# Kernel optimization log

Hardware: AMD Instinct MI355X
Metric: run time of the kernel (lower is better)

The kernel has to match this reference:

```python
import jax, jax.numpy as jnp
import numpy as np

B, CIN, L = 4, 128, 2048
D_MODEL, D_STATE, EXPAND, HEADDIM, NGROUPS = 256, 16, 3, 3, 1
D_INNER = EXPAND * D_MODEL            # 768
NHEADS = D_INNER // HEADDIM           # 256
CONV_DIM = D_INNER + 2 * NGROUPS * D_STATE   # 800
D_IN_PROJ = 2 * D_INNER + 2 * NGROUPS * D_STATE + NHEADS  # 1824
K_PROJ, D_CONV = 4, 4
EPS = 1e-5


def setup_inputs() -> dict:
    key = jax.random.key(0)
    ks = jax.random.split(key, 9)
    x = jax.random.normal(ks[0], (B, CIN, L), jnp.float32)
    proj_w = jax.random.normal(ks[1], (D_MODEL, CIN, K_PROJ), jnp.float32) / np.float32(np.sqrt(CIN * K_PROJ))
    in_proj_w = jax.random.normal(ks[2], (D_IN_PROJ, D_MODEL), jnp.float32) / np.float32(np.sqrt(D_MODEL))
    conv_w = jax.random.normal(ks[3], (CONV_DIM, 1, D_CONV), jnp.float32) / np.float32(np.sqrt(D_CONV))
    conv_b = jax.random.normal(ks[4], (CONV_DIM,), jnp.float32) * 0.01
    # dt_bias = inverse-softplus of dt ~ LogUniform[1e-3, 1e-1] (mamba2 init)
    u = jax.random.uniform(ks[5], (NHEADS,), jnp.float32)
    dt = jnp.exp(u * np.float32(np.log(0.1) - np.log(1e-3)) + np.float32(np.log(1e-3)))
    dt_bias = dt + jnp.log(-jnp.expm1(-dt))
    A_log = jnp.log(1.0 + 15.0 * jax.random.uniform(ks[6], (NHEADS,), jnp.float32))  # A in [-16,-1]
    D_skip = jnp.ones((NHEADS,), jnp.float32)
    norm_w = jnp.ones((D_INNER,), jnp.float32)
    out_proj_w = jax.random.normal(ks[7], (D_MODEL, D_INNER), jnp.float32) / np.float32(np.sqrt(D_INNER))
    return {"x": x, "proj_w": proj_w, "in_proj_w": in_proj_w, "conv_w": conv_w,
            "conv_b": conv_b, "dt_bias": dt_bias, "A_log": A_log, "D_skip": D_skip,
            "norm_w": norm_w, "out_proj_w": out_proj_w}


def _forward(x, proj_w, in_proj_w, conv_w, conv_b, dt_bias, A_log, D_skip, norm_w, out_proj_w):
    # outer Conv1d, padding='same' (k=4 -> left 1, right 2), no bias: (B,CIN,L)->(B,D_MODEL,L)
    h = jax.lax.conv_general_dilated(x, proj_w, (1,), [(1, 2)],
                                     dimension_numbers=("NCH", "OIH", "NCH"))
    u = h.transpose(0, 2, 1)                          # (B, L, d_model)
    zxbcdt = jnp.einsum("bld,ed->ble", u, in_proj_w)  # (B, L, 1824)
    z = zxbcdt[..., :D_INNER]                                     # (B,L,768)
    xBC = zxbcdt[..., D_INNER:D_INNER + CONV_DIM]                 # (B,L,800)
    dt = zxbcdt[..., D_INNER + CONV_DIM:]                         # (B,L,256)
    dt = jax.nn.softplus(dt + dt_bias)
    # depthwise causal conv (pad d_conv-1 on left) + SiLU
    xBC_c = jax.lax.conv_general_dilated(xBC.transpose(0, 2, 1), conv_w, (1,), [(D_CONV - 1, 0)],
                                         feature_group_count=CONV_DIM,
                                         dimension_numbers=("NCH", "OIH", "NCH"))
    xBC = jax.nn.silu(xBC_c + conv_b[None, :, None]).transpose(0, 2, 1)  # (B,L,800)
    xs = xBC[..., :D_INNER].reshape(B, L, NHEADS, HEADDIM)        # (B,L,H,P)
    Bm = xBC[..., D_INNER:D_INNER + D_STATE]                      # (B,L,N) (ngroups=1)
    Cm = xBC[..., D_INNER + D_STATE:]                             # (B,L,N)
    A = -jnp.exp(A_log)                                           # (H,)

    def step(hst, inp):
        dt_t, x_t, B_t, C_t = inp                 # (B,H),(B,H,P),(B,N),(B,N)
        dA = jnp.exp(dt_t * A)[:, :, None, None]  # (B,H,1,1)
        hst = dA * hst + jnp.einsum("bh,bhp,bn->bhpn", dt_t, x_t, B_t)
        y_t = jnp.einsum("bhpn,bn->bhp", hst, C_t)
        return hst, y_t

    h0 = jnp.zeros((B, NHEADS, HEADDIM, D_STATE), x.dtype)
    _, ys = jax.lax.scan(step, h0, (dt.transpose(1, 0, 2), xs.transpose(1, 0, 2, 3),
                                    Bm.transpose(1, 0, 2), Cm.transpose(1, 0, 2)))
    y = ys.transpose(1, 0, 2, 3) + D_skip[None, None, :, None] * xs   # (B,L,H,P)
    y = y.reshape(B, L, D_INNER)
    # gated RMSNorm: gate first, then normalize (norm_before_gate=False)
    y = y * jax.nn.silu(z)
    y = y * jax.lax.rsqrt(jnp.mean(y * y, axis=-1, keepdims=True) + EPS) * norm_w
    out = jnp.einsum("ble,de->bld", y, out_proj_w)   # (B,L,d_model)
    return out.transpose(0, 2, 1)                    # (B,d_model,L)


def reference(x, proj_w, in_proj_w, conv_w, conv_b, dt_bias, A_log, D_skip, norm_w, out_proj_w):
    return _forward(x, proj_w, in_proj_w, conv_w, conv_b, dt_bias, A_log, D_skip, norm_w, out_proj_w)
```

## Files before the change

### kernel.cpp

```cpp
#include <hip/hip_runtime.h>
#include <hip/hip_fp16.h>
#include <math.h>

#define B_     4
#define CIN    128
#define LEN    2048
#define DMODEL 256
#define DSTATE 16
#define NHEADS 256
#define DINNER 768
#define CONVDIM 800
#define DINPROJ 1824
#define EPS_   1e-5f
#define BAND   64
#define NBAND  32

typedef _Float16 f16x8 __attribute__((ext_vector_type(8)));
typedef _Float16 f16x4 __attribute__((ext_vector_type(4)));
typedef float    f32x4 __attribute__((ext_vector_type(4)));

__device__ __forceinline__ float silu_(float x){ return x / (1.0f + __expf(-x)); }
__device__ __forceinline__ float softplus_(float x){
    return x > 0.f ? x + log1pf(__expf(-x)) : log1pf(__expf(x));
}

__device__ __forceinline__ void gl2lds16(const _Float16* g, _Float16* l){
    __builtin_amdgcn_global_load_lds(
        (const __attribute__((address_space(1))) void*)g,
        (__attribute__((address_space(3))) void*)l, 16, 0, 0);
}

__global__ __launch_bounds__(256) void k_f2h(const float* __restrict__ a,
                                             _Float16* __restrict__ o, int n){
    for (int i = blockIdx.x * 256 + threadIdx.x; i < n; i += gridDim.x * 256)
        o[i] = (_Float16)a[i];
}

__global__ __launch_bounds__(256) void k_im2col(const float* __restrict__ x,
                                                _Float16* __restrict__ xcol){
    __shared__ float xs[CIN][68];
    int blk = blockIdx.x;
    int b  = blk >> 5;
    int l0 = (blk & 31) << 6;
    const float* xb = x + (size_t)b * CIN * LEN;
    for (int idx = threadIdx.x; idx < CIN * 67; idx += 256){
        int ci = idx / 67, j = idx % 67;
        int gl = l0 - 1 + j;
        xs[ci][j] = (gl >= 0 && gl < LEN) ? xb[ci * LEN + gl] : 0.f;
    }
    __syncthreads();
    #pragma unroll
    for (int v = 0; v < 16; v++){
        int id = v * 256 + threadIdx.x;
        int rl = id >> 6, c = id & 63;
        f16x8 pk;
        #pragma unroll
        for (int e = 0; e < 8; e++){
            int ci = c * 2 + (e >> 2), k = e & 3;
            pk[e] = (_Float16)xs[ci][rl + k];
        }
        *(f16x8*)&xcol[((size_t)(b * LEN + l0 + rl)) * 512 + c * 8] = pk;
    }
}

template<int K, int EPI>
__global__ __launch_bounds__(256) void k_gemm(const _Float16* __restrict__ A,
                                              const _Float16* __restrict__ Bw,
                                              const float* __restrict__ dt_bias,
                                              _Float16* __restrict__ o_u,
                                              _Float16* __restrict__ o_z,
                                              _Float16* __restrict__ o_xbc,
                                              _Float16* __restrict__ o_dt,
                                              float* __restrict__ o_f){
    __shared__ __align__(16) _Float16 As[128 * 32];
    __shared__ __align__(16) _Float16 Bs[128 * 32];
    int tid  = threadIdx.x;
    int wv   = tid >> 6;
    int lane = tid & 63;
    int quad = lane >> 4;
    int l16  = lane & 15;
    int m0 = blockIdx.x * 128;
    int n0 = blockIdx.y * 128;
    int wm = (wv >> 1) * 64;
    int wn = (wv & 1) * 64;
    int srow = lane >> 2;
    int scol = (lane & 3) * 8;

    f32x4 acc[4][4];
    #pragma unroll
    for (int i = 0; i < 4; i++)
        #pragma unroll
        for (int j = 0; j < 4; j++)
            acc[i][j] = (f32x4){0.f, 0.f, 0.f, 0.f};

    for (int k0 = 0; k0 < K; k0 += 32){
        #pragma unroll
        for (int j = 0; j < 2; j++){
            int ar = m0 + wv * 32 + j * 16 + srow;
            gl2lds16(A + (size_t)ar * K + k0 + scol,
                     &As[(wv * 32 + j * 16) * 32]);
            int nr = n0 + wv * 32 + j * 16 + srow;
            if (EPI == 1) nr = nr > (DINPROJ - 1) ? (DINPROJ - 1) : nr;
            gl2lds16(Bw + (size_t)nr * K + k0 + scol,
                     &Bs[(wv * 32 + j * 16) * 32]);
        }
        __syncthreads();
        f16x8 af[4], bf[4];
        #pragma unroll
        for (int i = 0; i < 4; i++)
            af[i] = *(const f16x8*)&As[(wm + i * 16 + l16) * 32 + quad * 8];
        #pragma unroll
        for (int j = 0; j < 4; j++)
            bf[j] = *(const f16x8*)&Bs[(wn + j * 16 + l16) * 32 + quad * 8];
        #pragma unroll
        for (int i = 0; i < 4; i++)
            #pragma unroll
            for (int j = 0; j < 4; j++)
                acc[i][j] = __builtin_amdgcn_mfma_f32_16x16x32_f16(
                                af[i], bf[j], acc[i][j], 0, 0, 0);
        __syncthreads();
    }

    if (EPI == 0){
        #pragma unroll
        for (int j = 0; j < 4; j++){
            int col = n0 + wn + j * 16 + l16;
            #pragma unroll
            for (int i = 0; i < 4; i++){
                int row = m0 + wm + i * 16 + quad * 4;
                #pragma unroll
                for (int r = 0; r < 4; r++)
                    o_u[(size_t)(row + r) * DMODEL + col] = (_Float16)acc[i][j][r];
            }
        }
    } else if (EPI == 1){
        #pragma unroll
        for (int j = 0; j < 4; j++){
            int col = n0 + wn + j * 16 + l16;
            if (col < DINNER){
                #pragma unroll
                for (int i = 0; i < 4; i++){
                    int row = m0 + wm + i * 16 + quad * 4;
                    #pragma unroll
                    for (int r = 0; r < 4; r++)
                        o_z[(size_t)(row + r) * DINNER + col] = (_Float16)acc[i][j][r];
                }
            } else if (col < DINNER + CONVDIM){
                int cc = col - DINNER;
                #pragma unroll
                for (int i = 0; i < 4; i++){
                    int row = m0 + wm + i * 16 + quad * 4;
                    #pragma unroll
                    for (int r = 0; r < 4; r++)
                        o_xbc[(size_t)(row + r) * CONVDIM + cc] = (_Float16)acc[i][j][r];
                }
            } else if (col < DINPROJ){
                int hh = col - (DINNER + CONVDIM);
                float bias = dt_bias[hh];
                #pragma unroll
                for (int i = 0; i < 4; i++){
                    int row = m0 + wm + i * 16 + quad * 4;
                    #pragma unroll
                    for (int r = 0; r < 4; r++)
                        o_dt[(size_t)(row + r) * NHEADS + hh] =
                            (_Float16)softplus_(acc[i][j][r] + bias);
                }
            }
        }
    } else {
        #pragma unroll
        for (int i = 0; i < 4; i++){
            int row = m0 + wm + i * 16 + quad * 4;
            int b = row >> 11, l = row & (LEN - 1);
            #pragma unroll
            for (int j = 0; j < 4; j++){
                int d = n0 + wn + j * 16 + l16;
                *(f32x4*)&o_f[(((size_t)(b * DMODEL + d)) << 11) + l] = acc[i][j];
            }
        }
    }
}

__global__ __launch_bounds__(256) void k_dwconv(const __half* __restrict__ xbc,
                                                const float* __restrict__ cw,
                                                const float* __restrict__ cb,
                                                __half* __restrict__ xcc){
    int idx = blockIdx.x * 256 + threadIdx.x;
    int c = idx % CONVDIM;
    int r = idx / CONVDIM;
    int l = r & (LEN - 1);
    float4 wv = *(const float4*)(cw + c * 4);
    float acc = cb[c];
    if (l >= 3){
        const __half* base = xbc + (size_t)(r - 3) * CONVDIM + c;
        acc += __half2float(base[0]) * wv.x + __half2float(base[CONVDIM]) * wv.y +
               __half2float(base[2 * CONVDIM]) * wv.z + __half2float(base[3 * CONVDIM]) * wv.w;
    } else {
        const float wk[4] = {wv.x, wv.y, wv.z, wv.w};
        for (int k = 0; k < 4; k++){
            int t = l - 3 + k;
            if (t >= 0) acc += __half2float(xbc[(size_t)(r + k - 3) * CONVDIM + c]) * wk[k];
        }
    }
    xcc[idx] = __float2half(silu_(acc));
}

__global__ __launch_bounds__(256) void k_y(const __half* __restrict__ dtb,
                                           const __half* __restrict__ xcc,
                                           const float* __restrict__ A_log,
                                           __half* __restrict__ y,
                                           float* __restrict__ E0,
                                           __half* __restrict__ cstate,
                                           float* __restrict__ dsum){
    __shared__ __align__(16) char smem[59392];
    __half* sBC = (__half*)smem;
    __half* sX  = (__half*)(smem + 4096);
    __half* sHL = (__half*)(smem + 4096);
    __half* sDT = (__half*)(smem + 28672);
    float*  sD  = (float*)(smem + 36864);
    float*  sG  = (float*)(smem + 54272);

    int band = blockIdx.x, hq = blockIdx.y, b = blockIdx.z;
    int row0 = band * BAND;
    int tid = threadIdx.x;
    int wv = tid >> 6, lane = tid & 63;

    {
        int c = wv, slot = c * 64 + lane;
        int row = slot >> 2, off = slot & 3;
        gl2lds16((const _Float16*)((const char*)xcc +
                   (size_t)(b * LEN + row0 + row) * 1600 + 1536 + off * 16),
                 (_Float16*)(smem + c * 1024));
    }
    #pragma unroll
    for (int i = 0; i < 6; i++){
        int c = wv + i * 4, slot = c * 64 + lane;
        int row = slot / 24, off = slot % 24;
        gl2lds16((const _Float16*)((const char*)xcc +
                   (size_t)(b * LEN + row0 + row) * 1600 + hq * 384 + off * 16),
                 (_Float16*)(smem + 4096 + c * 1024));
    }
    #pragma unroll
    for (int i = 0; i < 2; i++){
        int c = wv + i * 4, slot = c * 64 + lane;
        int row = slot >> 3, off = slot & 7;
        gl2lds16((const _Float16*)((const char*)dtb +
                   (size_t)(b * LEN + row0 + row) * 512 + hq * 128 + off * 16),
                 (_Float16*)(smem + 28672 + c * 1024));
    }
    __syncthreads();

    {
        int h = tid & 63, tb = tid >> 6;
        float A = -__expf(A_log[hq * 64 + h]);
        #pragma unroll
        for (int i = 0; i < 16; i++){
            int t = tb + i * 4;
            sD[t * 68 + h] = __expf(A * __half2float(sDT[t * 64 + h]));
        }
    }
    __syncthreads();

    if (tid < 64){
        int h = tid;
        float E = 1.f;
        float* ep = E0 + ((size_t)(b * LEN + row0)) * 256 + hq * 64 + h;
        for (int t = 0; t < 64; t++){
            E *= sD[t * 68 + h];
            *ep = E;
            ep += 256;
        }
        dsum[(size_t)(b * 256 + hq * 64 + h) * NBAND + band] = E;
    } else if (tid < 128){
        int tt = tid - 64;
        f16x8 ca = *(const f16x8*)&sBC[tt * 32 + 16];
        f16x8 cb = *(const f16x8*)&sBC[tt * 32 + 24];
        float cf[16];
        #pragma unroll
        for (int n = 0; n < 16; n++) cf[n] = (n < 8) ? (float)ca[n] : (float)cb[n - 8];
        for (int ss = 0; ss < 16; ss++){
            int s = (tt & 48) + ss;
            f16x8 ba = *(const f16x8*)&sBC[s * 32];
            f16x8 bb = *(const f16x8*)&sBC[s * 32 + 8];
            float acc = 0.f;
            #pragma unroll
            for (int n = 0; n < 8; n++)
                acc += cf[n] * (float)ba[n] + cf[n + 8] * (float)bb[n];
            sG[tt * 20 + ss] = acc;
        }
    } else {
        for (int idx = tid - 128; idx < 4096; idx += 128){
            int t = idx >> 6, h = idx & 63;
            float dtv = __half2float(sDT[t * 64 + h]);
            int xi = t * 192 + h * 3;
            sX[xi]     = __float2half(__half2float(sX[xi])     * dtv);
            sX[xi + 1] = __float2half(__half2float(sX[xi + 1]) * dtv);
            sX[xi + 2] = __float2half(__half2float(sX[xi + 2]) * dtv);
        }
    }
    __syncthreads();

    int t = tid >> 2, hsub = tid & 3, Hb = hsub * 16;
    int tmod = t & 15;
    float w[16], y0[16], y1[16], y2[16];
    #pragma unroll
    for (int i = 0; i < 16; i++){ w[i] = 1.f; y0[i] = 0.f; y1[i] = 0.f; y2[i] = 0.f; }

    for (int d = 0; d <= tmod; d++){
        int s = t - d;
        float g = sG[t * 20 + (tmod - d)];
        f32x4 Dv[4];
        #pragma unroll
        for (int k4 = 0; k4 < 4; k4++)
            Dv[k4] = *(const f32x4*)&sD[s * 68 + Hb + k4 * 4];
        f16x8 xv0 = *(const f16x8*)&sX[s * 192 + Hb * 3];
        f16x8 xv1 = *(const f16x8*)&sX[s * 192 + Hb * 3 + 8];
        f16x8 xv2 = *(const f16x8*)&sX[s * 192 + Hb * 3 + 16];
        f16x8 xv3 = *(const f16x8*)&sX[s * 192 + Hb * 3 + 24];
        f16x8 xv4 = *(const f16x8*)&sX[s * 192 + Hb * 3 + 32];
        f16x8 xv5 = *(const f16x8*)&sX[s * 192 + Hb * 3 + 40];
        #define XV(i) ((i)<8?(float)xv0[(i)]:(i)<16?(float)xv1[(i)-8]:(i)<24?(float)xv2[(i)-16]:\
                       (i)<32?(float)xv3[(i)-24]:(i)<40?(float)xv4[(i)-32]:(float)xv5[(i)-40])
        #pragma unroll
        for (int hh = 0; hh < 16; hh++){
            float wg = w[hh] * g;
            y0[hh] = fmaf(wg, XV(hh * 3 + 0), y0[hh]);
            y1[hh] = fmaf(wg, XV(hh * 3 + 1), y1[hh]);
            y2[hh] = fmaf(wg, XV(hh * 3 + 2), y2[hh]);
            w[hh] *= Dv[hh >> 2][hh & 3];
        }
        #undef XV
    }

    int h2 = tid >> 2, ng = tid & 3;
    float F[4][12];
    float vK[4];
    #pragma unroll
    for (int k = 0; k < 4; k++){
        #pragma unroll
        for (int i = 0; i < 12; i++) F[k][i] = 0.f;
        float v = 1.f;
        for (int ss = 15; ss >= 0; ss--){
            int s = k * 16 + ss;
            float x0 = __half2float(sX[s * 192 + h2 * 3]);
            float x1 = __half2float(sX[s * 192 + h2 * 3 + 1]);
            float x2 = __half2float(sX[s * 192 + h2 * 3 + 2]);
            f16x4 bv = *(const f16x4*)&sBC[s * 32 + ng * 4];
            #pragma unroll
            for (int nn = 0; nn < 4; nn++){
                float wb = v * (float)bv[nn];
                F[k][nn * 3 + 0] = fmaf(wb, x0, F[k][nn * 3 + 0]);
                F[k][nn * 3 + 1] = fmaf(wb, x1, F[k][nn * 3 + 1]);
                F[k][nn * 3 + 2] = fmaf(wb, x2, F[k][nn * 3 + 2]);
            }
            v *= sD[s * 68 + h2];
        }
        vK[k] = v;
    }

    __syncthreads();

    {
        float hc[12];
        #pragma unroll
        for (int i = 0; i < 12; i++) hc[i] = F[0][i];
        #pragma unroll
        for (int i = 0; i < 12; i++)
            sHL[(0 * 64 + h2) * 48 + ng * 12 + i] = __float2half(hc[i]);
        #pragma unroll
        for (int k = 1; k <= 2; k++){
            #pragma unroll
            for (int i = 0; i < 12; i++) hc[i] = fmaf(vK[k], hc[i], F[k][i]);
            #pragma unroll
            for (int i = 0; i < 12; i++)
                sHL[(k * 64 + h2) * 48 + ng * 12 + i] = __float2half(hc[i]);
        }
        __half* cp = cstate + ((size_t)((b * 256 + hq * 64 + h2) * NBAND + band)) * 48 + ng * 12;
        #pragma unroll
        for (int i = 0; i < 12; i++)
            cp[i] = __float2half(fmaf(vK[3], hc[i], F[3][i]));
    }
    __syncthreads();

    {
        f16x8 cva = *(const f16x8*)&sBC[t * 32 + 16];
        f16x8 cvb = *(const f16x8*)&sBC[t * 32 + 24];
        float cf[16];
        #pragma unroll
        for (int n = 0; n < 16; n++) cf[n] = (n < 8) ? (float)cva[n] : (float)cvb[n - 8];
        int k = t >> 4;
        if (k > 0){
            #pragma unroll
            for (int hh = 0; hh < 16; hh++){
                int h = Hb + hh;
                const __half* hl = &sHL[((k - 1) * 64 + h) * 48];
                f16x8 hv0 = *(const f16x8*)&hl[0];
                f16x8 hv1 = *(const f16x8*)&hl[8];
                f16x8 hv2 = *(const f16x8*)&hl[16];
                f16x8 hv3 = *(const f16x8*)&hl[24];
                f16x8 hv4 = *(const f16x8*)&hl[32];
                f16x8 hv5 = *(const f16x8*)&hl[40];
                #define HV(i) ((i)<8?(float)hv0[(i)]:(i)<16?(float)hv1[(i)-8]:(i)<24?(float)hv2[(i)-16]:\
                               (i)<32?(float)hv3[(i)-24]:(i)<40?(float)hv4[(i)-32]:(float)hv5[(i)-40])
                float a0 = 0.f, a1 = 0.f, a2 = 0.f;
                #pragma unroll
                for (int n = 0; n < 16; n++){
                    a0 = fmaf(cf[n], HV(n * 3 + 0), a0);
                    a1 = fmaf(cf[n], HV(n * 3 + 1), a1);
                    a2 = fmaf(cf[n], HV(n * 3 + 2), a2);
                }
                #undef HV
                y0[hh] = fmaf(w[hh], a0, y0[hh]);
                y1[hh] = fmaf(w[hh], a1, y1[hh]);
                y2[hh] = fmaf(w[hh], a2, y2[hh]);
            }
        }
        __half* yp = y + (size_t)(b * LEN + row0 + t) * DINNER + hq * 192 + hsub * 48;
        #pragma unroll
        for (int c = 0; c < 6; c++){
            f16x8 pk;
            #pragma unroll
            for (int e2 = 0; e2 < 8; e2++){
                int gi = c * 8 + e2;
                int hh = gi / 3, p = gi % 3;
                pk[e2] = (_Float16)(p == 0 ? y0[hh] : (p == 1 ? y1[hh] : y2[hh]));
            }
            *(f16x8*)&yp[c * 8] = pk;
        }
    }
}

__global__ __launch_bounds__(64) void k_scanB(__half* __restrict__ cstate,
                                              const float* __restrict__ dsum){
    int bh = blockIdx.x;
    int lane = threadIdx.x;
    if (lane >= 48) return;
    __half* st = cstate + (size_t)bh * NBAND * 48 + lane;
    const float* dd = dsum + (size_t)bh * NBAND;
    float H = 0.f;
    for (int c = 0; c < NBAND; c++){
        float d = dd[c];
        float s = __half2float(st[(size_t)c * 48]);
        st[(size_t)c * 48] = __float2half(H);
        H = fmaf(H, d, s);
    }
}

__global__ __launch_bounds__(256) void k_norm(__half* __restrict__ y,
                                              const __half* __restrict__ z,
                                              const __half* __restrict__ xcc,
                                              const float* __restrict__ E0,
                                              const __half* __restrict__ cstate,
                                              const float* __restrict__ D_skip,
                                              const float* __restrict__ nw){
    __shared__ __align__(16) char nsm[24576 + 64];
    __half* sHI = (__half*)nsm;
    float*  sCf = (float*)(nsm + 24576);
    __shared__ float wsum[4];
    int r = blockIdx.x;
    int b = r >> 11, l = r & (LEN - 1), band = l >> 6;
    int tid = threadIdx.x;
    int wv = tid >> 6, lane = tid & 63;

    #pragma unroll
    for (int i = 0; i < 6; i++){
        int chunk = (wv + i * 4) * 64 + lane;
        int head = chunk / 6, off = chunk % 6;
        gl2lds16((const _Float16*)((const char*)cstate +
                   ((size_t)(b * 256 + head) * NBAND + band) * 96 + off * 16),
                 (_Float16*)(nsm + (wv + i * 4) * 1024));
    }
    if (tid < 16)
        sCf[tid] = __half2float(xcc[(size_t)r * CONVDIM + DINNER + DSTATE + tid]);
    __syncthreads();

    const __half* zr = z + (size_t)r * DINNER;
    const __half* xr = xcc + (size_t)r * CONVDIM;
    const float*  er = E0 + (size_t)r * 256;
    __half* yr = y + (size_t)r * DINNER;
    float tv[3];
    #pragma unroll
    for (int q = 0; q < 3; q++){
        int e = tid + q * 256;
        int h = e / 3, p = e - h * 3;
        float corr = 0.f;
        #pragma unroll
        for (int n = 0; n < 16; n++)
            corr = fmaf(sCf[n], __half2float(sHI[h * 48 + n * 3 + p]), corr);
        float yf = __half2float(yr[e]) + er[h] * corr + D_skip[h] * __half2float(xr[e]);
        tv[q] = yf * silu_(__half2float(zr[e]));
    }
    float ss = tv[0] * tv[0] + tv[1] * tv[1] + tv[2] * tv[2];
    #pragma unroll
    for (int m = 1; m < 64; m <<= 1) ss += __shfl_xor(ss, m, 64);
    if ((tid & 63) == 0) wsum[tid >> 6] = ss;
    __syncthreads();
    float tot = wsum[0] + wsum[1] + wsum[2] + wsum[3];
    float sc = rsqrtf(tot / (float)DINNER + EPS_);
    #pragma unroll
    for (int q = 0; q < 3; q++){
        int e = tid + q * 256;
        yr[e] = __float2half(tv[q] * sc * nw[e]);
    }
}

extern "C" void kernel_launch(void* const* d_in, const int* in_sizes, int n_in,
                              void* d_out, int out_size, void* d_ws, size_t ws_size,
                              hipStream_t stream) {
    const float* x          = (const float*)d_in[0];
    const float* proj_w     = (const float*)d_in[1];
    const float* in_proj_w  = (const float*)d_in[2];
    const float* conv_w     = (const float*)d_in[3];
    const float* conv_b     = (const float*)d_in[4];
    const float* dt_bias    = (const float*)d_in[5];
    const float* A_log      = (const float*)d_in[6];
    const float* D_skip     = (const float*)d_in[7];
    const float* norm_w     = (const float*)d_in[8];
    const float* out_proj_w = (const float*)d_in[9];
    float* out = (float*)d_out;

    char* ob = (char*)d_out;
    _Float16* pw_h  = (_Float16*)ob;
    _Float16* ipw_h = (_Float16*)(ob + 262144);
    float*    E0    = (float*)d_out;

    char* wsb = (char*)d_ws;
    _Float16* xcol  = (_Float16*)(wsb);
    _Float16* u_h   = (_Float16*)(wsb + 8388608);
    __half*   xcc_h = (__half*)(wsb);
    __half*   z_h   = (__half*)(wsb + 13107200);
    __half*   xbc_h = (__half*)(wsb + 25690112);
    __half*   y_h   = xbc_h;
    __half*   dt_h  = (__half*)(wsb + 38797312);
    __half*   cstate= (__half*)(wsb + 42991616);
    float*    dsum  = (float*)(wsb + 46137344);
    _Float16* opw_h = (_Float16*)(wsb + 46268416);

    k_f2h   <<<64, 256, 0, stream>>>(proj_w,     pw_h,  DMODEL * CIN * 4);
    k_f2h   <<<64, 256, 0, stream>>>(in_proj_w,  ipw_h, DINPROJ * DMODEL);
    k_f2h   <<<64, 256, 0, stream>>>(out_proj_w, opw_h, DMODEL * DINNER);
    k_im2col<<<128, 256, 0, stream>>>(x, xcol);
    k_gemm<512, 0><<<dim3(64, 2), 256, 0, stream>>>(xcol, pw_h, nullptr,
        u_h, nullptr, nullptr, nullptr, nullptr);
    k_gemm<256, 1><<<dim3(64, 15), 256, 0, stream>>>(u_h, ipw_h, dt_bias,
        nullptr, (_Float16*)z_h, (_Float16*)xbc_h, (_Float16*)dt_h, nullptr);
    k_dwconv<<<25600, 256, 0, stream>>>(xbc_h, conv_w, conv_b, xcc_h);
    k_y     <<<dim3(NBAND, 4, B_), 256, 0, stream>>>(dt_h, xcc_h, A_log,
                                                     y_h, E0, cstate, dsum);
    k_scanB <<<1024, 64, 0, stream>>>(cstate, dsum);
    k_norm  <<<8192, 256, 0, stream>>>(y_h, z_h, xcc_h, E0, cstate,
                                       D_skip, norm_w);
    k_gemm<768, 2><<<dim3(64, 2), 256, 0, stream>>>((const _Float16*)y_h, opw_h,
        nullptr, nullptr, nullptr, nullptr, nullptr, out);
}
```

Baseline: 289.2 us.

## Fuse weight casts, vectorize dwconv, batch norm rows, stage out-proj stores

Merges the three weight-conversion launches into one kernel and halves the im2col tile so twice as many blocks run. The depthwise conv now handles 8 channels per thread with 16-byte vector loads and stores. The norm kernel processes 16 rows per block, so the cstate slice is loaded into LDS once per 16 rows instead of per row. The final GEMM transposes its output through LDS to write coalesced contiguous rows of the (B,d,L) output. These changes aim to cut launch overhead and uncoalesced memory traffic, at the cost of fewer blocks and extra barriers in the norm and GEMM epilogue.

```diff
diff --git a/kernel.cpp b/kernel.cpp
--- a/kernel.cpp
+++ b/kernel.cpp
@@ -30,27 +30,36 @@
         (__attribute__((address_space(3))) void*)l, 16, 0, 0);
 }
 
-__global__ __launch_bounds__(256) void k_f2h(const float* __restrict__ a,
-                                             _Float16* __restrict__ o, int n){
-    for (int i = blockIdx.x * 256 + threadIdx.x; i < n; i += gridDim.x * 256)
-        o[i] = (_Float16)a[i];
+__global__ __launch_bounds__(256) void k_f2h3(const float* __restrict__ a0,
+                                              _Float16* __restrict__ o0, int n0,
+                                              const float* __restrict__ a1,
+                                              _Float16* __restrict__ o1, int n1,
+                                              const float* __restrict__ a2,
+                                              _Float16* __restrict__ o2, int n2){
+    int stride = gridDim.x * 256;
+    for (int i = blockIdx.x * 256 + threadIdx.x; i < n0; i += stride)
+        o0[i] = (_Float16)a0[i];
+    for (int i = blockIdx.x * 256 + threadIdx.x; i < n1; i += stride)
+        o1[i] = (_Float16)a1[i];
+    for (int i = blockIdx.x * 256 + threadIdx.x; i < n2; i += stride)
+        o2[i] = (_Float16)a2[i];
 }
 
 __global__ __launch_bounds__(256) void k_im2col(const float* __restrict__ x,
                                                 _Float16* __restrict__ xcol){
-    __shared__ float xs[CIN][68];
+    __shared__ float xs[CIN][36];
     int blk = blockIdx.x;
-    int b  = blk >> 5;
-    int l0 = (blk & 31) << 6;
+    int b  = blk >> 6;
+    int l0 = (blk & 63) << 5;
     const float* xb = x + (size_t)b * CIN * LEN;
-    for (int idx = threadIdx.x; idx < CIN * 67; idx += 256){
-        int ci = idx / 67, j = idx % 67;
+    for (int idx = threadIdx.x; idx < CIN * 35; idx += 256){
+        int ci = idx / 35, j = idx % 35;
         int gl = l0 - 1 + j;
         xs[ci][j] = (gl >= 0 && gl < LEN) ? xb[ci * LEN + gl] : 0.f;
     }
     __syncthreads();
     #pragma unroll
-    for (int v = 0; v < 16; v++){
+    for (int v = 0; v < 8; v++){
         int id = v * 256 + threadIdx.x;
         int rl = id >> 6, c = id & 63;
         f16x8 pk;
@@ -168,15 +177,26 @@
             }
         }
     } else {
-        #pragma unroll
-        for (int i = 0; i < 4; i++){
-            int row = m0 + wm + i * 16 + quad * 4;
-            int b = row >> 11, l = row & (LEN - 1);
-            #pragma unroll
-            for (int j = 0; j < 4; j++){
-                int d = n0 + wn + j * 16 + l16;
-                *(f32x4*)&o_f[(((size_t)(b * DMODEL + d)) << 11) + l] = acc[i][j];
+        float* tbuf = (float*)As;
+        int bb = m0 >> 11, ll0 = m0 & (LEN - 1);
+        for (int s = 0; s < 8; s++){
+            __syncthreads();
+            int j = (wn == 0) ? s : s - 4;
+            if (j >= 0 && j < 4){
+                #pragma unroll
+                for (int i = 0; i < 4; i++){
+                    int row = wm + i * 16 + quad * 4;
+                    *(f32x4*)&tbuf[l16 * 128 + row] = acc[i][j];
+                }
             }
+            __syncthreads();
+            int dc = tid >> 4, ch = tid & 15;
+            float* op = o_f + (((size_t)(bb * DMODEL + n0 + s * 16 + dc)) << 11)
+                            + ll0 + ch * 8;
+            f32x4 v0 = *(const f32x4*)&tbuf[dc * 128 + ch * 8];
+            f32x4 v1 = *(const f32x4*)&tbuf[dc * 128 + ch * 8 + 4];
+            *(f32x4*)&op[0] = v0;
+            *(f32x4*)&op[4] = v1;
         }
     }
 }
@@ -186,23 +206,34 @@
                                                 const float* __restrict__ cb,
                                                 __half* __restrict__ xcc){
     int idx = blockIdx.x * 256 + threadIdx.x;
-    int c = idx % CONVDIM;
-    int r = idx / CONVDIM;
+    int g = idx % 100;
+    int r = idx / 100;
     int l = r & (LEN - 1);
-    float4 wv = *(const float4*)(cw + c * 4);
-    float acc = cb[c];
-    if (l >= 3){
-        const __half* base = xbc + (size_t)(r - 3) * CONVDIM + c;
-        acc += __half2float(base[0]) * wv.x + __half2float(base[CONVDIM]) * wv.y +
-               __half2float(base[2 * CONVDIM]) * wv.z + __half2float(base[3 * CONVDIM]) * wv.w;
-    } else {
-        const float wk[4] = {wv.x, wv.y, wv.z, wv.w};
-        for (int k = 0; k < 4; k++){
-            int t = l - 3 + k;
-            if (t >= 0) acc += __half2float(xbc[(size_t)(r + k - 3) * CONVDIM + c]) * wk[k];
-        }
-    }
-    xcc[idx] = __float2half(silu_(acc));
+    int c0 = g * 8;
+    float4 wv[8];
+    float acc[8];
+    #pragma unroll
+    for (int e = 0; e < 8; e++){
+        wv[e] = *(const float4*)(cw + (c0 + e) * 4);
+        acc[e] = cb[c0 + e];
+    }
+    const __half* base = xbc + (size_t)r * CONVDIM + c0;
+    #pragma unroll
+    for (int k = 0; k < 4; k++){
+        if (l + k >= 3){
+            f16x8 v = *(const f16x8*)(base + ((ptrdiff_t)k - 3) * CONVDIM);
+            #pragma unroll
+            for (int e = 0; e < 8; e++){
+                float wk = (k == 0) ? wv[e].x : (k == 1) ? wv[e].y
+                         : (k == 2) ? wv[e].z : wv[e].w;
+                acc[e] = fmaf((float)v[e], wk, acc[e]);
+            }
+        }
+    }
+    f16x8 o;
+    #pragma unroll
+    for (int e = 0; e < 8; e++) o[e] = (_Float16)silu_(acc[e]);
+    *(f16x8*)(xcc + (size_t)r * CONVDIM + c0) = o;
 }
 
 __global__ __launch_bounds__(256) void k_y(const __half* __restrict__ dtb,
@@ -453,12 +484,14 @@
                                               const __half* __restrict__ cstate,
                                               const float* __restrict__ D_skip,
                                               const float* __restrict__ nw){
-    __shared__ __align__(16) char nsm[24576 + 64];
+    __shared__ __align__(16) char nsm[24576 + 1024];
     __half* sHI = (__half*)nsm;
     float*  sCf = (float*)(nsm + 24576);
     __shared__ float wsum[4];
-    int r = blockIdx.x;
-    int b = r >> 11, l = r & (LEN - 1), band = l >> 6;
+    int rb = blockIdx.x;
+    int b = rb >> 7, g16 = rb & 127;
+    int r0 = g16 << 4;
+    int band = r0 >> 6;
     int tid = threadIdx.x;
     int wv = tid >> 6, lane = tid & 63;
 
@@ -470,37 +503,53 @@
                    ((size_t)(b * 256 + head) * NBAND + band) * 96 + off * 16),
                  (_Float16*)(nsm + (wv + i * 4) * 1024));
     }
-    if (tid < 16)
-        sCf[tid] = __half2float(xcc[(size_t)r * CONVDIM + DINNER + DSTATE + tid]);
+    {
+        int row16 = tid >> 4, n = tid & 15;
+        sCf[tid] = __half2float(
+            xcc[(size_t)(b * LEN + r0 + row16) * CONVDIM + DINNER + DSTATE + n]);
+    }
     __syncthreads();
 
-    const __half* zr = z + (size_t)r * DINNER;
-    const __half* xr = xcc + (size_t)r * CONVDIM;
-    const float*  er = E0 + (size_t)r * 256;
-    __half* yr = y + (size_t)r * DINNER;
-    float tv[3];
+    int hq_[3], pq_[3];
+    float dskq[3], nwq[3];
     #pragma unroll
     for (int q = 0; q < 3; q++){
         int e = tid + q * 256;
-        int h = e / 3, p = e - h * 3;
-        float corr = 0.f;
-        #pragma unroll
-        for (int n = 0; n < 16; n++)
-            corr = fmaf(sCf[n], __half2float(sHI[h * 48 + n * 3 + p]), corr);
-        float yf = __half2float(yr[e]) + er[h] * corr + D_skip[h] * __half2float(xr[e]);
-        tv[q] = yf * silu_(__half2float(zr[e]));
-    }
-    float ss = tv[0] * tv[0] + tv[1] * tv[1] + tv[2] * tv[2];
-    #pragma unroll
-    for (int m = 1; m < 64; m <<= 1) ss += __shfl_xor(ss, m, 64);
-    if ((tid & 63) == 0) wsum[tid >> 6] = ss;
-    __syncthreads();
-    float tot = wsum[0] + wsum[1] + wsum[2] + wsum[3];
-    float sc = rsqrtf(tot / (float)DINNER + EPS_);
-    #pragma unroll
-    for (int q = 0; q < 3; q++){
-        int e = tid + q * 256;
-        yr[e] = __float2half(tv[q] * sc * nw[e]);
+        hq_[q] = e / 3; pq_[q] = e - hq_[q] * 3;
+        dskq[q] = D_skip[hq_[q]];
+        nwq[q] = nw[e];
+    }
+
+    for (int row = 0; row < 16; row++){
+        size_t r = (size_t)(b * LEN + r0 + row);
+        const __half* zr = z + r * DINNER;
+        const __half* xr = xcc + r * CONVDIM;
+        const float*  er = E0 + r * 256;
+        __half* yr = y + r * DINNER;
+        float tv[3];
+        #pragma unroll
+        for (int q = 0; q < 3; q++){
+            int e = tid + q * 256;
+            int h = hq_[q], p = pq_[q];
+            float corr = 0.f;
+            #pragma unroll
+            for (int n = 0; n < 16; n++)
+                corr = fmaf(sCf[row * 16 + n],
+                            __half2float(sHI[h * 48 + n * 3 + p]), corr);
+            float yf = __half2float(yr[e]) + er[h] * corr + dskq[q] * __half2float(xr[e]);
+            tv[q] = yf * silu_(__half2float(zr[e]));
+        }
+        float ss = tv[0] * tv[0] + tv[1] * tv[1] + tv[2] * tv[2];
+        #pragma unroll
+        for (int m = 1; m < 64; m <<= 1) ss += __shfl_xor(ss, m, 64);
+        if ((tid & 63) == 0) wsum[tid >> 6] = ss;
+        __syncthreads();
+        float tot = wsum[0] + wsum[1] + wsum[2] + wsum[3];
+        float sc = rsqrtf(tot / (float)DINNER + EPS_);
+        #pragma unroll
+        for (int q = 0; q < 3; q++)
+            yr[tid + q * 256] = __float2half(tv[q] * sc * nwq[q]);
+        __syncthreads();
     }
 }
 
@@ -536,20 +585,20 @@
     float*    dsum  = (float*)(wsb + 46137344);
     _Float16* opw_h = (_Float16*)(wsb + 46268416);
 
-    k_f2h   <<<64, 256, 0, stream>>>(proj_w,     pw_h,  DMODEL * CIN * 4);
-    k_f2h   <<<64, 256, 0, stream>>>(in_proj_w,  ipw_h, DINPROJ * DMODEL);
-    k_f2h   <<<64, 256, 0, stream>>>(out_proj_w, opw_h, DMODEL * DINNER);
-    k_im2col<<<128, 256, 0, stream>>>(x, xcol);
+    k_f2h3  <<<128, 256, 0, stream>>>(proj_w, pw_h, DMODEL * CIN * 4,
+                                      in_proj_w, ipw_h, DINPROJ * DMODEL,
+                                      out_proj_w, opw_h, DMODEL * DINNER);
+    k_im2col<<<256, 256, 0, stream>>>(x, xcol);
     k_gemm<512, 0><<<dim3(64, 2), 256, 0, stream>>>(xcol, pw_h, nullptr,
         u_h, nullptr, nullptr, nullptr, nullptr);
     k_gemm<256, 1><<<dim3(64, 15), 256, 0, stream>>>(u_h, ipw_h, dt_bias,
         nullptr, (_Float16*)z_h, (_Float16*)xbc_h, (_Float16*)dt_h, nullptr);
-    k_dwconv<<<25600, 256, 0, stream>>>(xbc_h, conv_w, conv_b, xcc_h);
+    k_dwconv<<<3200, 256, 0, stream>>>(xbc_h, conv_w, conv_b, xcc_h);
     k_y     <<<dim3(NBAND, 4, B_), 256, 0, stream>>>(dt_h, xcc_h, A_log,
                                                      y_h, E0, cstate, dsum);
     k_scanB <<<1024, 64, 0, stream>>>(cstate, dsum);
-    k_norm  <<<8192, 256, 0, stream>>>(y_h, z_h, xcc_h, E0, cstate,
-                                       D_skip, norm_w);
+    k_norm  <<<512, 256, 0, stream>>>(y_h, z_h, xcc_h, E0, cstate,
+                                      D_skip, norm_w);
     k_gemm<768, 2><<<dim3(64, 2), 256, 0, stream>>>((const _Float16*)y_h, opw_h,
         nullptr, nullptr, nullptr, nullptr, nullptr, out);
 }
```

Result: slower. 345.4 us (+19.4%).
